# Kernel optimization log

Measured on AMD Instinct MI355X. Metric: run time of the kernel, lower is better.

## Reference

```python
import jax, jax.numpy as jnp
import numpy as np

T, D_IN, D_OUT, E = 8192, 1024, 1024, 8
LN_EPS = 1e-5


def setup_inputs() -> dict:
    key = jax.random.key(0)
    k1, k2, k3 = jax.random.split(key, 3)
    x = jax.random.normal(k1, (T, D_IN), dtype=jnp.float32)
    # tokens are pre-sorted by expert; equal load => capacity = T // E per expert
    expert_frequency = jnp.full((E,), T // E, dtype=jnp.int64)
    # per-expert Linear(input_dim, output_dim) params
    W = jax.random.normal(k2, (E, D_IN, D_OUT), dtype=jnp.float32) / np.sqrt(D_IN)
    b = jax.random.normal(k3, (E, D_OUT), dtype=jnp.float32) * 0.02
    # per-expert LayerNorm(output_dim) affine params
    ln_gamma = jnp.ones((E, D_OUT), dtype=jnp.float32)
    ln_beta = jnp.zeros((E, D_OUT), dtype=jnp.float32)
    return {
        "expert_ordered_input": x,
        "expert_frequency": expert_frequency,
        "W": W,
        "b": b,
        "ln_gamma": ln_gamma,
        "ln_beta": ln_beta,
    }


def reference(expert_ordered_input, expert_frequency, W, b, ln_gamma, ln_beta):
    # Grouped-GEMM form of: split tokens by expert_frequency, apply per-expert
    # LayerBlock (Linear -> relu -> LayerNorm), then concat along token dim.
    # Frequencies are equal (capacity = T // E), so the ragged split is a reshape.
    x = expert_ordered_input
    n_tok, d_in = x.shape
    n_exp = W.shape[0]
    cap = n_tok // n_exp  # static capacity per expert
    xe = x.reshape(n_exp, cap, d_in)                       # [E, cap, d_in]
    h = jnp.einsum("ecd,edf->ecf", xe, W) + b[:, None, :]  # [E, cap, d_out]
    h = jax.nn.relu(h)
    mu = jnp.mean(h, axis=-1, keepdims=True)
    var = jnp.var(h, axis=-1, keepdims=True)
    hn = (h - mu) * jax.lax.rsqrt(var + LN_EPS)
    out = hn * ln_gamma[:, None, :] + ln_beta[:, None, :]
    return out.reshape(n_tok, -1)                          # concat over experts
```

## Files before the change

kernel.cpp:

```cpp
#include <hip/hip_runtime.h>
#include <hip/hip_bf16.h>
#include <stdint.h>

#define T_TOK 8192
#define DIN   1024
#define DOUT  1024
#define NEXP  8
#define CAP   1024
#define LN_EPS 1e-5f

typedef __attribute__((ext_vector_type(8))) short short8;
typedef __attribute__((ext_vector_type(4))) float f32x4;

__device__ __forceinline__ unsigned short f2bf(float f) {
    union { float f; unsigned int u; } v; v.f = f;
    unsigned int u = v.u;
    unsigned int r = u + 0x7FFFu + ((u >> 16) & 1u);
    return (unsigned short)(r >> 16);
}

__global__ __launch_bounds__(256) void wt_kernel(const float* __restrict__ W,
                                                 unsigned short* __restrict__ Wt) {
    __shared__ float tile[32][33];
    int t  = blockIdx.x;
    int e  = t >> 10;
    int k0 = ((t >> 5) & 31) * 32;
    int n0 = (t & 31) * 32;
    int tid = threadIdx.x;
    const float* Wp = W + (size_t)e * DIN * DOUT;
    unsigned short* Wtp = Wt + (size_t)e * DIN * DOUT;
    {
        int k  = tid >> 3;
        int c4 = tid & 7;
        float4 v = *(const float4*)(Wp + (size_t)(k0 + k) * DOUT + n0 + c4 * 4);
        tile[k][c4 * 4 + 0] = v.x; tile[k][c4 * 4 + 1] = v.y;
        tile[k][c4 * 4 + 2] = v.z; tile[k][c4 * 4 + 3] = v.w;
    }
    __syncthreads();
    {
        int n  = tid >> 3;
        int kc = tid & 7;
        ushort4 o;
        o.x = f2bf(tile[kc * 4 + 0][n]);
        o.y = f2bf(tile[kc * 4 + 1][n]);
        o.z = f2bf(tile[kc * 4 + 2][n]);
        o.w = f2bf(tile[kc * 4 + 3][n]);
        *(ushort4*)(Wtp + (size_t)(n0 + n) * DIN + k0 + kc * 4) = o;
    }
}

__global__ __launch_bounds__(512, 2) void gemmln_kernel(
    const float* __restrict__ X,
    const unsigned short* __restrict__ Wt,
    const float* __restrict__ Bias,
    const float* __restrict__ G,
    const float* __restrict__ Bt,
    float* __restrict__ Out)
{
    __shared__ unsigned short As[32 * 1024];

    int blk = blockIdx.x;
    int tid = threadIdx.x;
    int e   = blk & 7;
    int m0  = (blk >> 3) * 32;

    int wave = tid >> 6;
    int lane = tid & 63;
    int lrow = lane & 15;
    int quad = lane >> 4;
    int wn   = wave * 128;

    const float* Xe = X + (size_t)(e * CAP + m0) * DIN;
    const unsigned short* We = Wt + (size_t)e * DOUT * DIN;

#pragma unroll
    for (int it = 0; it < 16; it++) {
        int f  = it * 512 + tid;
        int r  = f >> 8;
        int c4 = f & 255;
        float4 v = ((const float4*)Xe)[f];
        ushort4 o;
        o.x = f2bf(v.x); o.y = f2bf(v.y); o.z = f2bf(v.z); o.w = f2bf(v.w);
        int O    = c4 >> 1;
        int half = c4 & 1;
        int O2   = O ^ (r & 7);
        *(ushort4*)&As[r * 1024 + O2 * 8 + half * 4] = o;
    }
    __syncthreads();

    f32x4 acc[2][8];
#pragma unroll
    for (int i = 0; i < 2; i++)
#pragma unroll
        for (int j = 0; j < 8; j++)
            acc[i][j] = (f32x4)(0.0f);

#pragma unroll 2
    for (int k0 = 0; k0 < DIN; k0 += 32) {
        short8 bf[8];
#pragma unroll
        for (int j = 0; j < 8; j++) {
            int n = wn + j * 16 + lrow;
            bf[j] = *(const short8*)(We + (size_t)n * DIN + k0 + quad * 8);
        }
        short8 af[2];
#pragma unroll
        for (int i = 0; i < 2; i++) {
            int r  = i * 16 + lrow;
            int O2 = ((k0 >> 3) + quad) ^ (r & 7);
            af[i] = *(const short8*)&As[r * 1024 + O2 * 8];
        }
#pragma unroll
        for (int j = 0; j < 8; j++) {
            acc[0][j] = __builtin_amdgcn_mfma_f32_16x16x32_bf16(af[0], bf[j], acc[0][j], 0, 0, 0);
            acc[1][j] = __builtin_amdgcn_mfma_f32_16x16x32_bf16(af[1], bf[j], acc[1][j], 0, 0, 0);
        }
    }

    float bias[8], gg[8], bb[8];
#pragma unroll
    for (int j = 0; j < 8; j++) {
        int col = e * DOUT + wn + j * 16 + lrow;
        bias[j] = Bias[col];
        gg[j]   = G[col];
        bb[j]   = Bt[col];
    }

    __syncthreads();
    float2* lnp = (float2*)As;
    float2* mrs = ((float2*)As) + 256;

#pragma unroll
    for (int i = 0; i < 2; i++) {
#pragma unroll
        for (int r = 0; r < 4; r++) {
            float s = 0.f, ss = 0.f;
#pragma unroll
            for (int j = 0; j < 8; j++) {
                float v = fmaxf(acc[i][j][r] + bias[j], 0.f);
                acc[i][j][r] = v;
                s += v;
                ss = fmaf(v, v, ss);
            }
#pragma unroll
            for (int m = 1; m <= 8; m <<= 1) {
                s  += __shfl_xor(s, m);
                ss += __shfl_xor(ss, m);
            }
            if (lrow == 0)
                lnp[(i * 16 + quad * 4 + r) * 8 + wave] = make_float2(s, ss);
        }
    }
    __syncthreads();
    if (tid < 32) {
        float s = 0.f, ss = 0.f;
#pragma unroll
        for (int w = 0; w < 8; w++) {
            float2 p = lnp[tid * 8 + w];
            s += p.x; ss += p.y;
        }
        float mu  = s * (1.0f / DOUT);
        float var = fmaxf(ss * (1.0f / DOUT) - mu * mu, 0.f);
        mrs[tid] = make_float2(mu, rsqrtf(var + LN_EPS));
    }
    __syncthreads();

#pragma unroll
    for (int i = 0; i < 2; i++) {
#pragma unroll
        for (int r = 0; r < 4; r++) {
            int lr = i * 16 + quad * 4 + r;
            float2 m = mrs[lr];
            size_t grow = (size_t)(e * CAP + m0 + lr);
#pragma unroll
            for (int j = 0; j < 8; j++) {
                int gcol = wn + j * 16 + lrow;
                Out[grow * DOUT + gcol] = (acc[i][j][r] - m.x) * m.y * gg[j] + bb[j];
            }
        }
    }
}

extern "C" void kernel_launch(void* const* d_in, const int* in_sizes, int n_in,
                              void* d_out, int out_size, void* d_ws, size_t ws_size,
                              hipStream_t stream) {
    const float* x  = (const float*)d_in[0];
    const float* W  = (const float*)d_in[2];
    const float* b  = (const float*)d_in[3];
    const float* g  = (const float*)d_in[4];
    const float* be = (const float*)d_in[5];
    float* out = (float*)d_out;

    const size_t WT_BYTES = (size_t)NEXP * DIN * DOUT * 2;
    if (ws_size < WT_BYTES) return;

    unsigned short* Wt = (unsigned short*)d_ws;

    wt_kernel<<<dim3(8192), dim3(256), 0, stream>>>(W, Wt);
    gemmln_kernel<<<dim3(256), dim3(512), 0, stream>>>(x, Wt, b, g, be, out);
}
```

Before: 171.7 us.

## Split into prep, tiled 128x128 GEMM with LDS direct loads, and LayerNorm kernels

Replaces the fused 32-row GEMM+LayerNorm kernel with three kernels. A prep kernel converts X to bf16 and transposes W. A 128x128-tiled GEMM uses global_load_lds to stage A and B through LDS, then writes bf16 relu activations and per-chunk partial sums. A separate LN kernel reduces those partials and normalizes. The aim is better operand reuse than the old design, which streamed B straight from global memory, at the cost of extra HBM round-trips for Xb, Hb and the partials, an additional launch, and rounding the activations to bf16 before normalization.

```diff
diff --git a/kernel.cpp b/kernel.cpp
--- a/kernel.cpp
+++ b/kernel.cpp
@@ -9,6 +9,10 @@
 #define CAP   1024
 #define LN_EPS 1e-5f
 
+#define BM 128
+#define BN 128
+#define BK 32
+
 typedef __attribute__((ext_vector_type(8))) short short8;
 typedef __attribute__((ext_vector_type(4))) float f32x4;
 
@@ -18,125 +22,145 @@
     unsigned int r = u + 0x7FFFu + ((u >> 16) & 1u);
     return (unsigned short)(r >> 16);
 }
-
-__global__ __launch_bounds__(256) void wt_kernel(const float* __restrict__ W,
-                                                 unsigned short* __restrict__ Wt) {
+__device__ __forceinline__ float bf2f(unsigned short h) {
+    union { unsigned int u; float f; } v; v.u = ((unsigned int)h) << 16;
+    return v.f;
+}
+
+__device__ __forceinline__ void gld16(void* l, const void* g) {
+    __builtin_amdgcn_global_load_lds(
+        (const __attribute__((address_space(1))) unsigned int*)(uintptr_t)g,
+        (__attribute__((address_space(3))) unsigned int*)(uintptr_t)l,
+        16, 0, 0);
+}
+
+__global__ __launch_bounds__(256) void prep_kernel(
+    const float* __restrict__ X, const float* __restrict__ W,
+    unsigned short* __restrict__ Xb, unsigned short* __restrict__ Wt) {
     __shared__ float tile[32][33];
-    int t  = blockIdx.x;
-    int e  = t >> 10;
-    int k0 = ((t >> 5) & 31) * 32;
-    int n0 = (t & 31) * 32;
+    int blk = blockIdx.x;
     int tid = threadIdx.x;
-    const float* Wp = W + (size_t)e * DIN * DOUT;
-    unsigned short* Wtp = Wt + (size_t)e * DIN * DOUT;
-    {
-        int k  = tid >> 3;
-        int c4 = tid & 7;
-        float4 v = *(const float4*)(Wp + (size_t)(k0 + k) * DOUT + n0 + c4 * 4);
-        tile[k][c4 * 4 + 0] = v.x; tile[k][c4 * 4 + 1] = v.y;
-        tile[k][c4 * 4 + 2] = v.z; tile[k][c4 * 4 + 3] = v.w;
-    }
-    __syncthreads();
-    {
-        int n  = tid >> 3;
-        int kc = tid & 7;
+    if (blk < 8192) {
+        int e = blk & 7;
+        int r = blk >> 3;
+        size_t i = ((size_t)(e * CAP + r)) * 256 + tid;
+        float4 v = ((const float4*)X)[i];
         ushort4 o;
-        o.x = f2bf(tile[kc * 4 + 0][n]);
-        o.y = f2bf(tile[kc * 4 + 1][n]);
-        o.z = f2bf(tile[kc * 4 + 2][n]);
-        o.w = f2bf(tile[kc * 4 + 3][n]);
-        *(ushort4*)(Wtp + (size_t)(n0 + n) * DIN + k0 + kc * 4) = o;
-    }
-}
-
-__global__ __launch_bounds__(512, 2) void gemmln_kernel(
-    const float* __restrict__ X,
+        o.x = f2bf(v.x); o.y = f2bf(v.y); o.z = f2bf(v.z); o.w = f2bf(v.w);
+        ((ushort4*)Xb)[i] = o;
+    } else {
+        int t  = blk - 8192;
+        int e  = t & 7;
+        int tl = t >> 3;
+        int k0 = (tl >> 5) * 32;
+        int n0 = (tl & 31) * 32;
+        const float* Wp = W + (size_t)e * DIN * DOUT;
+        unsigned short* Wtp = Wt + (size_t)e * DIN * DOUT;
+        {
+            int k  = tid >> 3;
+            int c4 = tid & 7;
+            float4 v = *(const float4*)(Wp + (size_t)(k0 + k) * DOUT + n0 + c4 * 4);
+            tile[k][c4 * 4 + 0] = v.x; tile[k][c4 * 4 + 1] = v.y;
+            tile[k][c4 * 4 + 2] = v.z; tile[k][c4 * 4 + 3] = v.w;
+        }
+        __syncthreads();
+        {
+            int n  = tid >> 3;
+            int kc = tid & 7;
+            ushort4 o;
+            o.x = f2bf(tile[kc * 4 + 0][n]);
+            o.y = f2bf(tile[kc * 4 + 1][n]);
+            o.z = f2bf(tile[kc * 4 + 2][n]);
+            o.w = f2bf(tile[kc * 4 + 3][n]);
+            *(ushort4*)(Wtp + (size_t)(n0 + n) * DIN + k0 + kc * 4) = o;
+        }
+    }
+}
+
+__global__ __launch_bounds__(256, 2) void gemm5_kernel(
+    const unsigned short* __restrict__ Xb,
     const unsigned short* __restrict__ Wt,
     const float* __restrict__ Bias,
-    const float* __restrict__ G,
-    const float* __restrict__ Bt,
-    float* __restrict__ Out)
+    unsigned short* __restrict__ Hb,
+    float2* __restrict__ P)
 {
-    __shared__ unsigned short As[32 * 1024];
+    __shared__ unsigned short As[4][BM * BK];
+    __shared__ unsigned short Bs[4][BN * BK];
 
     int blk = blockIdx.x;
-    int tid = threadIdx.x;
     int e   = blk & 7;
-    int m0  = (blk >> 3) * 32;
-
+    int mi  = blk >> 6;
+    int m0  = mi * BM;
+    int ni  = (blk >> 3) & 7;
+    int n0  = ni * BN;
+
+    int tid  = threadIdx.x;
     int wave = tid >> 6;
     int lane = tid & 63;
+    int wm   = (wave >> 1) * 64;
+    int wn   = (wave & 1) * 64;
     int lrow = lane & 15;
     int quad = lane >> 4;
-    int wn   = wave * 128;
-
-    const float* Xe = X + (size_t)(e * CAP + m0) * DIN;
-    const unsigned short* We = Wt + (size_t)e * DOUT * DIN;
-
-#pragma unroll
-    for (int it = 0; it < 16; it++) {
-        int f  = it * 512 + tid;
-        int r  = f >> 8;
-        int c4 = f & 255;
-        float4 v = ((const float4*)Xe)[f];
-        ushort4 o;
-        o.x = f2bf(v.x); o.y = f2bf(v.y); o.z = f2bf(v.z); o.w = f2bf(v.w);
-        int O    = c4 >> 1;
-        int half = c4 & 1;
-        int O2   = O ^ (r & 7);
-        *(ushort4*)&As[r * 1024 + O2 * 8 + half * 4] = o;
-    }
-    __syncthreads();
-
-    f32x4 acc[2][8];
-#pragma unroll
-    for (int i = 0; i < 2; i++)
-#pragma unroll
-        for (int j = 0; j < 8; j++)
+
+    const unsigned short* Ag = Xb + (size_t)(e * CAP + m0) * DIN;
+    const unsigned short* Bg = Wt + (size_t)e * DOUT * DIN + (size_t)n0 * DIN;
+
+    int l0 = tid;
+    int l1 = tid + 256;
+    int ar0 = l0 >> 2, ac0 = (l0 & 3) * 8;
+    int ar1 = l1 >> 2, ac1 = (l1 & 3) * 8;
+
+    f32x4 acc[4][4];
+#pragma unroll
+    for (int i = 0; i < 4; i++)
+#pragma unroll
+        for (int j = 0; j < 4; j++)
             acc[i][j] = (f32x4)(0.0f);
 
-#pragma unroll 2
-    for (int k0 = 0; k0 < DIN; k0 += 32) {
-        short8 bf[8];
-#pragma unroll
-        for (int j = 0; j < 8; j++) {
-            int n = wn + j * 16 + lrow;
-            bf[j] = *(const short8*)(We + (size_t)n * DIN + k0 + quad * 8);
-        }
-        short8 af[2];
-#pragma unroll
-        for (int i = 0; i < 2; i++) {
-            int r  = i * 16 + lrow;
-            int O2 = ((k0 >> 3) + quad) ^ (r & 7);
-            af[i] = *(const short8*)&As[r * 1024 + O2 * 8];
-        }
-#pragma unroll
-        for (int j = 0; j < 8; j++) {
-            acc[0][j] = __builtin_amdgcn_mfma_f32_16x16x32_bf16(af[0], bf[j], acc[0][j], 0, 0, 0);
-            acc[1][j] = __builtin_amdgcn_mfma_f32_16x16x32_bf16(af[1], bf[j], acc[1][j], 0, 0, 0);
-        }
-    }
-
-    float bias[8], gg[8], bb[8];
-#pragma unroll
-    for (int j = 0; j < 8; j++) {
-        int col = e * DOUT + wn + j * 16 + lrow;
-        bias[j] = Bias[col];
-        gg[j]   = G[col];
-        bb[j]   = Bt[col];
-    }
-
-    __syncthreads();
-    float2* lnp = (float2*)As;
-    float2* mrs = ((float2*)As) + 256;
-
-#pragma unroll
-    for (int i = 0; i < 2; i++) {
+    for (int kb = 0; kb < DIN; kb += 4 * BK) {
+#pragma unroll
+        for (int s = 0; s < 4; s++) {
+            int k0 = kb + s * BK;
+            gld16(&As[s][l0 * 8], Ag + (size_t)ar0 * DIN + k0 + ac0);
+            gld16(&As[s][l1 * 8], Ag + (size_t)ar1 * DIN + k0 + ac1);
+            gld16(&Bs[s][l0 * 8], Bg + (size_t)ar0 * DIN + k0 + ac0);
+            gld16(&Bs[s][l1 * 8], Bg + (size_t)ar1 * DIN + k0 + ac1);
+        }
+        __syncthreads();
+
+#pragma unroll
+        for (int s = 0; s < 4; s++) {
+            short8 af[4], bf[4];
+#pragma unroll
+            for (int i = 0; i < 4; i++)
+                af[i] = *(const short8*)&As[s][(wm + i * 16 + lrow) * BK + quad * 8];
+#pragma unroll
+            for (int j = 0; j < 4; j++)
+                bf[j] = *(const short8*)&Bs[s][(wn + j * 16 + lrow) * BK + quad * 8];
+#pragma unroll
+            for (int i = 0; i < 4; i++)
+#pragma unroll
+                for (int j = 0; j < 4; j++)
+                    acc[i][j] = __builtin_amdgcn_mfma_f32_16x16x32_bf16(af[i], bf[j], acc[i][j], 0, 0, 0);
+        }
+        __syncthreads();
+    }
+
+    float bias[4];
+#pragma unroll
+    for (int j = 0; j < 4; j++)
+        bias[j] = Bias[e * DOUT + n0 + wn + j * 16 + lrow];
+
+    int tok0  = e * CAP + m0 + wm;
+    int chunk = ni * 2 + (wave & 1);
+
+#pragma unroll
+    for (int i = 0; i < 4; i++) {
 #pragma unroll
         for (int r = 0; r < 4; r++) {
             float s = 0.f, ss = 0.f;
 #pragma unroll
-            for (int j = 0; j < 8; j++) {
+            for (int j = 0; j < 4; j++) {
                 float v = fmaxf(acc[i][j][r] + bias[j], 0.f);
                 acc[i][j][r] = v;
                 s += v;
@@ -147,38 +171,58 @@
                 s  += __shfl_xor(s, m);
                 ss += __shfl_xor(ss, m);
             }
+            int grow = tok0 + i * 16 + quad * 4 + r;
             if (lrow == 0)
-                lnp[(i * 16 + quad * 4 + r) * 8 + wave] = make_float2(s, ss);
+                P[(size_t)grow * 16 + chunk] = make_float2(s, ss);
+#pragma unroll
+            for (int j = 0; j < 4; j++) {
+                int gcol = n0 + wn + j * 16 + lrow;
+                Hb[(size_t)grow * DOUT + gcol] = f2bf(acc[i][j][r]);
+            }
+        }
+    }
+}
+
+__global__ __launch_bounds__(256) void ln2_kernel(
+    const unsigned short* __restrict__ Hb,
+    const float2* __restrict__ P,
+    const float* __restrict__ G,
+    const float* __restrict__ Bt,
+    float* __restrict__ Out)
+{
+    int blk = blockIdx.x;
+    int e   = blk & 7;
+    int row = e * CAP + (blk >> 3);
+    int tid = threadIdx.x;
+    __shared__ float sh[2];
+
+    if (tid < 16) {
+        float2 p = P[(size_t)row * 16 + tid];
+        float s = p.x, ss = p.y;
+#pragma unroll
+        for (int m = 1; m <= 8; m <<= 1) {
+            s  += __shfl_xor(s, m);
+            ss += __shfl_xor(ss, m);
+        }
+        if (tid == 0) {
+            float mu  = s * (1.0f / DOUT);
+            float var = fmaxf(ss * (1.0f / DOUT) - mu * mu, 0.f);
+            sh[0] = mu;
+            sh[1] = rsqrtf(var + LN_EPS);
         }
     }
     __syncthreads();
-    if (tid < 32) {
-        float s = 0.f, ss = 0.f;
-#pragma unroll
-        for (int w = 0; w < 8; w++) {
-            float2 p = lnp[tid * 8 + w];
-            s += p.x; ss += p.y;
-        }
-        float mu  = s * (1.0f / DOUT);
-        float var = fmaxf(ss * (1.0f / DOUT) - mu * mu, 0.f);
-        mrs[tid] = make_float2(mu, rsqrtf(var + LN_EPS));
-    }
-    __syncthreads();
-
-#pragma unroll
-    for (int i = 0; i < 2; i++) {
-#pragma unroll
-        for (int r = 0; r < 4; r++) {
-            int lr = i * 16 + quad * 4 + r;
-            float2 m = mrs[lr];
-            size_t grow = (size_t)(e * CAP + m0 + lr);
-#pragma unroll
-            for (int j = 0; j < 8; j++) {
-                int gcol = wn + j * 16 + lrow;
-                Out[grow * DOUT + gcol] = (acc[i][j][r] - m.x) * m.y * gg[j] + bb[j];
-            }
-        }
-    }
+    float mu = sh[0], rs = sh[1];
+
+    ushort4 hb = ((const ushort4*)Hb)[(size_t)row * 256 + tid];
+    float4 g = ((const float4*)G)[e * 256 + tid];
+    float4 b = ((const float4*)Bt)[e * 256 + tid];
+    float4 y;
+    y.x = (bf2f(hb.x) - mu) * rs * g.x + b.x;
+    y.y = (bf2f(hb.y) - mu) * rs * g.y + b.y;
+    y.z = (bf2f(hb.z) - mu) * rs * g.z + b.z;
+    y.w = (bf2f(hb.w) - mu) * rs * g.w + b.w;
+    ((float4*)Out)[(size_t)row * 256 + tid] = y;
 }
 
 extern "C" void kernel_launch(void* const* d_in, const int* in_sizes, int n_in,
@@ -192,10 +236,18 @@
     float* out = (float*)d_out;
 
     const size_t WT_BYTES = (size_t)NEXP * DIN * DOUT * 2;
-    if (ws_size < WT_BYTES) return;
+    const size_t XB_BYTES = (size_t)T_TOK * DIN * 2;
+    const size_t P_BYTES  = (size_t)T_TOK * 16 * 8;
+    const size_t HB_BYTES = (size_t)T_TOK * DOUT * 2;
+    if (ws_size < WT_BYTES + XB_BYTES + P_BYTES + HB_BYTES) return;
 
     unsigned short* Wt = (unsigned short*)d_ws;
-
-    wt_kernel<<<dim3(8192), dim3(256), 0, stream>>>(W, Wt);
-    gemmln_kernel<<<dim3(256), dim3(512), 0, stream>>>(x, Wt, b, g, be, out);
-}
+    unsigned short* Xb = (unsigned short*)((char*)d_ws + WT_BYTES);
+    float2* P = (float2*)((char*)d_ws + WT_BYTES + XB_BYTES);
+    unsigned short* Hb = (unsigned short*)((char*)d_ws + WT_BYTES + XB_BYTES + P_BYTES);
+
+    dim3 tb(256);
+    prep_kernel<<<dim3(16384), tb, 0, stream>>>(x, W, Xb, Wt);
+    gemm5_kernel<<<dim3(512), tb, 0, stream>>>(Xb, Wt, b, Hb, P);
+    ln2_kernel<<<dim3(8192), tb, 0, stream>>>(Hb, P, g, be, out);
+}
```

Result: faster. 152.0 us (-11.5%).
